# Optimization experiments

Measured on AMD Instinct MI355X. Metric: run time of the kernel, lower is better.

## Reference

```python
import jax, jax.numpy as jnp
import numpy as np

# Config matching init_kwargs / module defaults
B_T2I, B_LM, B_MMU = 2, 2, 2
B = B_T2I + B_LM + B_MMU
S = 1280
H, D = 16, 64
IMAGE_BE = [(128, 1152)]          # t2i_image_begin_end
MMU_END = 1027
PAD_BE = [(0, 80), (0, 100), (0, 110), (0, 0)]  # create_block_mask default pad_begin_ends


def _mixed_mask():
    """Vectorized translation of OmniAttentionMechanism.mixed_mask -> bool [B,S,S]."""
    q = jnp.arange(S)[:, None]    # [S,1] query index
    kv = jnp.arange(S)[None, :]   # [1,S] key index

    # t2i_full_begin / t2i_full_end (per-q image block bounds)
    full_begin = jnp.arange(S)
    full_end = jnp.arange(S)
    for ib, ie in IMAGE_BE:
        full_begin = full_begin.at[ib:ie].set(ib)
        full_end = full_end.at[ib:ie].set(ie)

    # pad_ends[b, kv]: arange baseline, first len(PAD_BE) batches get pad region end
    pad_ends = jnp.tile(jnp.arange(S)[None, :], (B, 1))
    for cnt, (pb, pe) in enumerate(PAD_BE):
        pad_ends = pad_ends.at[cnt, pb:pe].set(pe)

    # t2i: padded-causal OR bidirectional image block
    causal = (~(kv < pad_ends[:, None, :]) & (q >= kv)) | (q == kv)   # [B,S,S]
    full = (kv < full_end[:, None]) & (kv >= full_begin[:, None])     # [S,S] (q-indexed bounds)
    t2i = causal | full[None]
    lm = (q >= kv)[None]                                              # [1,S,S]
    mmu = ((q >= kv) | (kv < MMU_END))[None]                          # [1,S,S]

    b = jnp.arange(B)[:, None, None]
    # Faithful to the original XOR composition (terms are batch-disjoint so == OR)
    return ((b < B_T2I) & t2i) ^ ((b >= B_T2I) & (b < B_T2I + B_LM) & lm) ^ ((b >= B_T2I + B_LM) & mmu)


def setup_inputs() -> dict:
    key = jax.random.key(0)
    kq, kk, kv = jax.random.split(key, 3)
    shape = (B, H, S, D)
    return {
        "q": jax.random.normal(kq, shape, dtype=jnp.float32),
        "k": jax.random.normal(kk, shape, dtype=jnp.float32),
        "v": jax.random.normal(kv, shape, dtype=jnp.float32),
    }


def reference(q, k, v):
    """flex_attention(q, k, v, block_mask=mixed-t2i-lm-mmu) equivalent."""
    mask = _mixed_mask()[:, None]  # [B,1,S,S], broadcast over heads
    scale = 1.0 / jnp.sqrt(jnp.float32(D))  # flex_attention default scale
    scores = jnp.einsum('bhqd,bhkd->bhqk', q, k) * scale
    scores = jnp.where(mask, scores, -jnp.inf)  # every row has >=1 allowed key (q==kv / q>=kv)
    attn = jax.nn.softmax(scores, axis=-1)
    return jnp.einsum('bhqk,bhkd->bhqd', attn, v)
```

## Files before the change

### kernel.cpp

```cpp
#include <hip/hip_runtime.h>
#include <hip/hip_bf16.h>
#include <math.h>


#define SS 1280
#define DD 64
#define NH 16
#define TK 64
#define QB 128
#define NITEMS 960

typedef __attribute__((ext_vector_type(8))) short bf16x8;
typedef __attribute__((ext_vector_type(16))) float f32x16;

union UA { uint u[4]; bf16x8 v; };

__device__ inline uint pk2(float a, float b) {
    union { __hip_bfloat162 h; uint u; } cv;
    cv.h = __float22bfloat162_rn(float2{a, b});
    return cv.u;
}

__device__ inline void pl32(uint& a, uint& b) {
    asm volatile("v_permlane32_swap_b32 %0, %1" : "+v"(a), "+v"(b));
}

#define WAITVM4() asm volatile("s_waitcnt vmcnt(4)" ::: "memory")
#define WAITVM0() asm volatile("s_waitcnt vmcnt(0)" ::: "memory")

__device__ inline void decode_item(int i, int& b, int& h, int& qt) {
    if (i < 96)  { qt = 9; b = i / 16; h = i % 16; return; }
    i -= 96;
    if (i < 256) { b = i / 128; qt = 1 + (i % 128) / 16; h = i % 16; return; }
    i -= 256;
    if (i < 32)  { b = 2 + i / 16; qt = 8; h = i % 16; return; }
    i -= 32;
    if (i < 32)  { b = 4 + i / 16; qt = 8; h = i % 16; return; }
    i -= 32;
    if (i < 256) { b = 4 + i / 128; qt = (i % 128) / 16; h = i % 16; return; }
    i -= 256;
    if (i < 224) { qt = 7 - i / 32; b = 2 + (i % 32) / 16; h = i % 16; return; }
    i -= 224;
    if (i < 32)  { b = 2 + i / 16; qt = 0; h = i % 16; return; }
    i -= 32;
    b = i / 16; qt = 0; h = i % 16;
}

__global__ void zero_ctr_kernel(int* ctr) { if (threadIdx.x == 0) *ctr = 0; }

__global__ __launch_bounds__(256) void prepass8(
    const float* __restrict__ K, const float* __restrict__ V,
    ushort* __restrict__ Kb, ushort* __restrict__ Vtb)
{
    const int gx = blockIdx.x;
    const int t  = threadIdx.x;
    if (gx < 3840) {
        const size_t e = ((size_t)gx * 256 + t) * 8;
        const float4 a = *(const float4*)(K + e);
        const float4 c = *(const float4*)(K + e + 4);
        UA u;
        u.u[0] = pk2(a.x, a.y); u.u[1] = pk2(a.z, a.w);
        u.u[2] = pk2(c.x, c.y); u.u[3] = pk2(c.z, c.w);
        *(bf16x8*)(Kb + e) = u.v;
    } else {
        const int g   = gx - 3840;
        const int kvt = g % 20;
        const int p   = g / 20;
        __shared__ float T[64 * 67];
        const float* src = V + (size_t)p * (SS * DD) + (size_t)(kvt * 64) * DD;
#pragma unroll
        for (int i = 0; i < 16; ++i) {
            const int idx = t + 256 * i;
            T[(idx >> 6) * 67 + (idx & 63)] = src[idx];
        }
        __syncthreads();
        ushort* dst = Vtb + (size_t)p * (DD * SS) + kvt * 64;
#pragma unroll
        for (int i = 0; i < 2; ++i) {
            const int c0 = t + 256 * i;
            const int d = c0 >> 3, kc = c0 & 7;
            UA u;
#pragma unroll
            for (int j = 0; j < 4; ++j)
                u.u[j] = pk2(T[(kc * 8 + 2 * j) * 67 + d], T[(kc * 8 + 2 * j + 1) * 67 + d]);
            *(bf16x8*)(dst + (size_t)d * SS + kc * 8) = u.v;
        }
    }
}

__global__ __launch_bounds__(256) void omni_attn12(
    const float* __restrict__ Q, const ushort* __restrict__ Kb,
    const ushort* __restrict__ Vtb, float* __restrict__ O, int* __restrict__ ctr)
{
    const int t   = threadIdx.x;
    const int w   = t >> 6;
    const int l   = t & 63;
    const int l31 = l & 31;
    const int hi2 = l >> 5;

    __shared__ char smem[49152];
    __shared__ int s_item;

    const float scale = 0.125f * 1.44269504088896340736f;

    int koff[2], voff[2];
#pragma unroll
    for (int rd = 0; rd < 2; ++rd) {
        const int ci  = rd * 256 + w * 64 + l;
        const int row = ci >> 3, cc = ci & 7;
        koff[rd] = row * DD + (cc ^ (row & 7)) * 8;
        const int d = ci >> 3, vc = ci & 7;
        voff[rd] = d * SS + (vc ^ ((d ^ (d >> 3)) & 7)) * 8;
    }

    for (;;) {
        if (t == 0) s_item = atomicAdd(ctr, 1);
        __syncthreads();
        const int item = s_item;
        if (item >= NITEMS) break;

        int b, h, qt;
        decode_item(item, b, h, qt);
        const int p   = b * NH + h;
        const int qb0 = qt * QB;
        const int qw0 = qb0 + w * 32;
        const int qr  = qw0 + l31;
        const size_t pbase = (size_t)p * (SS * DD);

        const int bt = (b < 2) ? 0 : (b < 4) ? 1 : 2;
        const int pe = (b == 0) ? 80 : (b == 1) ? 100 : 0;
        const int qmax_blk = qb0 + QB - 1;
        const int qmax_w   = qw0 + 31;
        const bool blk_img = (qb0 + QB - 1 >= 128) && (qb0 < 1152);
        const bool w_img   = (qw0 >= 128) && (qw0 < 1152);

        bf16x8 qf[4];
#pragma unroll
        for (int ks = 0; ks < 4; ++ks) {
            const float* src = Q + pbase + (size_t)qr * DD + ks * 16 + hi2 * 8;
            const float4 a = *(const float4*)(src);
            const float4 c = *(const float4*)(src + 4);
            UA u;
            u.u[0] = pk2(a.x, a.y); u.u[1] = pk2(a.z, a.w);
            u.u[2] = pk2(c.x, c.y); u.u[3] = pk2(c.z, c.w);
            qf[ks] = u.v;
        }
        __builtin_amdgcn_sched_barrier(0);

        f32x16 o_acc[2];
#pragma unroll
        for (int ntd = 0; ntd < 2; ++ntd)
#pragma unroll
            for (int r = 0; r < 16; ++r) o_acc[ntd][r] = 0.f;
        float psum = 0.f;

        auto need_blk = [&](int k0) -> bool {
            if (bt == 0) return (k0 <= qmax_blk) || (blk_img && k0 >= 128 && k0 < 1152);
            if (bt == 1) return (k0 <= qmax_blk);
            return (k0 <= qmax_blk) || (k0 < 1027);
        };
        auto next_tile = [&](int k) -> int {
            k += TK;
            while (k < SS && !need_blk(k)) k += TK;
            return k;
        };
        auto stage = [&](int bsel, int k0) {
            char* buf = smem + bsel * 16384;
            const ushort* Kp = Kb + pbase + (size_t)k0 * DD;
            const ushort* Vp = Vtb + pbase + k0;
#pragma unroll
            for (int rd = 0; rd < 2; ++rd) {
                char* lb = buf + (rd * 256 + w * 64) * 16;
                __builtin_amdgcn_global_load_lds(
                    (const __attribute__((address_space(1))) void*)(Kp + koff[rd]),
                    (__attribute__((address_space(3))) void*)lb, 16, 0, 0);
            }
#pragma unroll
            for (int rd = 0; rd < 2; ++rd) {
                char* lb = buf + 8192 + (rd * 256 + w * 64) * 16;
                __builtin_amdgcn_global_load_lds(
                    (const __attribute__((address_space(1))) void*)(Vp + voff[rd]),
                    (__attribute__((address_space(3))) void*)lb, 16, 0, 0);
            }
        };

        int ka = 0, cur = 0;
        int kb = next_tile(0);
        int kc = (kb < SS) ? next_tile(kb) : SS;
        stage(0, ka);
        if (kb < SS) { stage(1, kb); WAITVM4(); } else { WAITVM0(); }
        __builtin_amdgcn_s_barrier();
        __builtin_amdgcn_sched_barrier(0);

        while (true) {
            if (kc < SS) stage((cur + 2) % 3, kc);

            char* cbuf = smem + cur * 16384;
            const int k0 = ka;
            const bool kv_img = (k0 >= 128) && (k0 < 1152);
            bool need_w, full_w;
            if (bt == 0) {
                need_w = (k0 <= qmax_w) || (w_img && kv_img);
                full_w = ((k0 >= pe) && (k0 + 63 <= qw0)) || (w_img && kv_img);
            } else if (bt == 1) {
                need_w = (k0 <= qmax_w);
                full_w = (k0 + 63 <= qw0);
            } else {
                need_w = (k0 <= qmax_w) || (k0 < 1027);
                full_w = (k0 + 63 <= qw0) || (k0 + 63 < 1027);
            }

            if (need_w) {
#pragma unroll
                for (int nt = 0; nt < 2; ++nt) {
                    f32x16 s;
#pragma unroll
                    for (int r = 0; r < 16; ++r) s[r] = 0.f;
                    __builtin_amdgcn_s_setprio(1);
#pragma unroll
                    for (int ksd = 0; ksd < 4; ++ksd) {
                        const int row = nt * 32 + l31;
                        int off = row * 128 + ksd * 32 + hi2 * 16;
                        off ^= (row & 7) << 4;
                        const bf16x8 kf = *(const bf16x8*)(cbuf + off);
                        s = __builtin_amdgcn_mfma_f32_32x32x16_bf16(kf, qf[ksd], s, 0, 0, 0);
                    }
                    __builtin_amdgcn_s_setprio(0);

                    const int c0 = k0 + nt * 32;
                    uint c[8];
#pragma unroll
                    for (int i = 0; i < 8; ++i) {
                        float pa, pb;
                        if (full_w) {
                            pa = __builtin_amdgcn_exp2f(s[2 * i] * scale);
                            pb = __builtin_amdgcn_exp2f(s[2 * i + 1] * scale);
                        } else {
                            const int r0i = 2 * i, r1i = 2 * i + 1;
                            const int kva = c0 + (r0i & 3) + 8 * (r0i >> 2) + 4 * hi2;
                            const int kvb = c0 + (r1i & 3) + 8 * (r1i >> 2) + 4 * hi2;
                            bool aa, ab;
                            if (bt == 0) {
                                aa = (qr == kva) | ((kva >= pe) & (qr >= kva)) |
                                     ((qr >= 128) & (qr < 1152) & (kva >= 128) & (kva < 1152));
                                ab = (qr == kvb) | ((kvb >= pe) & (qr >= kvb)) |
                                     ((qr >= 128) & (qr < 1152) & (kvb >= 128) & (kvb < 1152));
                            } else if (bt == 1) {
                                aa = (qr >= kva); ab = (qr >= kvb);
                            } else {
                                aa = (qr >= kva) | (kva < 1027);
                                ab = (qr >= kvb) | (kvb < 1027);
                            }
                            pa = aa ? __builtin_amdgcn_exp2f(s[2 * i] * scale) : 0.f;
                            pb = ab ? __builtin_amdgcn_exp2f(s[2 * i + 1] * scale) : 0.f;
                        }
                        psum += pa + pb;
                        c[i] = pk2(pa, pb);
                    }

                    UA A0, A1;
                    {
                        uint a0 = c[0], b0 = c[2]; pl32(a0, b0);
                        uint a1 = c[1], b1 = c[3]; pl32(a1, b1);
                        A0.u[0] = a0; A0.u[1] = a1; A0.u[2] = b0; A0.u[3] = b1;
                        uint a2 = c[4], b2 = c[6]; pl32(a2, b2);
                        uint a3 = c[5], b3 = c[7]; pl32(a3, b3);
                        A1.u[0] = a2; A1.u[1] = a3; A1.u[2] = b2; A1.u[3] = b3;
                    }

                    __builtin_amdgcn_s_setprio(1);
#pragma unroll
                    for (int ntd = 0; ntd < 2; ++ntd) {
                        const int row = ntd * 32 + l31;
                        const int swz = ((row ^ (row >> 3)) & 7) << 4;
                        int off0 = 8192 + row * 128 + (2 * nt) * 32 + hi2 * 16;     off0 ^= swz;
                        int off1 = 8192 + row * 128 + (2 * nt + 1) * 32 + hi2 * 16; off1 ^= swz;
                        const bf16x8 vf0 = *(const bf16x8*)(cbuf + off0);
                        o_acc[ntd] = __builtin_amdgcn_mfma_f32_32x32x16_bf16(A0.v, vf0, o_acc[ntd], 0, 0, 0);
                        const bf16x8 vf1 = *(const bf16x8*)(cbuf + off1);
                        o_acc[ntd] = __builtin_amdgcn_mfma_f32_32x32x16_bf16(A1.v, vf1, o_acc[ntd], 0, 0, 0);
                    }
                    __builtin_amdgcn_s_setprio(0);
                }
            }

            if (kc < SS) { WAITVM4(); } else { WAITVM0(); }
            __builtin_amdgcn_s_barrier();
            __builtin_amdgcn_sched_barrier(0);
            if (kb >= SS) break;
            ka = kb; kb = kc; kc = (kc < SS) ? next_tile(kc) : SS;
            cur = (cur + 1) % 3;
        }

        psum += __shfl_xor(psum, 32, 64);
#pragma unroll
        for (int r = 0; r < 16; ++r) {
            const int q_loc = (r & 3) + 8 * (r >> 2) + 4 * hi2;
            const float tv = __shfl(psum, q_loc, 64);
            const float iv = 1.f / tv;
            float* dst = O + pbase + (size_t)(qw0 + q_loc) * DD + l31;
#pragma unroll
            for (int ntd = 0; ntd < 2; ++ntd)
                dst[ntd * 32] = o_acc[ntd][r] * iv;
        }
    }
}

extern "C" void kernel_launch(void* const* d_in, const int* in_sizes, int n_in,
                              void* d_out, int out_size, void* d_ws, size_t ws_size,
                              hipStream_t stream) {
    const float* q = (const float*)d_in[0];
    const float* k = (const float*)d_in[1];
    const float* v = (const float*)d_in[2];
    float* o = (float*)d_out;

    const size_t NE = 7864320ULL;
    ushort* Kb  = (ushort*)d_ws;
    ushort* Vtb = Kb + NE;
    int* ctr    = (int*)((char*)d_ws + 2 * NE * sizeof(ushort));

    zero_ctr_kernel<<<1, 64, 0, stream>>>(ctr);
    prepass8<<<dim3(5760), 256, 0, stream>>>(k, v, Kb, Vtb);
    omni_attn12<<<dim3(768), 256, 0, stream>>>(q, Kb, Vtb, o, ctr);
}
```

Before: 114.8 us.

## Load V fragments directly to registers and drop persistent atomic scheduler

V tiles are now read straight from global memory into registers per wave, so LDS staging covers only K. This halves shared memory and adds occupancy hints (launch_bounds 256,4). The persistent work-stealing loop with its atomic counter and zero-init kernel is replaced by one block per work item in the same decode order, which also removes one kernel launch. The cost is more VGPRs for the V fragments and possibly less coalesced, higher-latency V loads. The pipeline also always issues a K stage, using a dummy tile at the end, to keep the vmcnt accounting uniform.

Result: slower. 143.0 us (+24.6%).

```diff
diff --git a/kernel.cpp b/kernel.cpp
--- a/kernel.cpp
+++ b/kernel.cpp
@@ -25,8 +25,7 @@
     asm volatile("v_permlane32_swap_b32 %0, %1" : "+v"(a), "+v"(b));
 }
 
-#define WAITVM4() asm volatile("s_waitcnt vmcnt(4)" ::: "memory")
-#define WAITVM0() asm volatile("s_waitcnt vmcnt(0)" ::: "memory")
+#define WAITVM2() asm volatile("s_waitcnt vmcnt(2)" ::: "memory")
 
 __device__ inline void decode_item(int i, int& b, int& h, int& qt) {
     if (i < 96)  { qt = 9; b = i / 16; h = i % 16; return; }
@@ -45,8 +44,6 @@
     i -= 32;
     b = i / 16; qt = 0; h = i % 16;
 }
-
-__global__ void zero_ctr_kernel(int* ctr) { if (threadIdx.x == 0) *ctr = 0; }
 
 __global__ __launch_bounds__(256) void prepass8(
     const float* __restrict__ K, const float* __restrict__ V,
@@ -67,11 +64,10 @@
         const int kvt = g % 20;
         const int p   = g / 20;
         __shared__ float T[64 * 67];
-        const float* src = V + (size_t)p * (SS * DD) + (size_t)(kvt * 64) * DD;
 #pragma unroll
         for (int i = 0; i < 16; ++i) {
             const int idx = t + 256 * i;
-            T[(idx >> 6) * 67 + (idx & 63)] = src[idx];
+            T[(idx >> 6) * 67 + (idx & 63)] = V[(size_t)p * (SS * DD) + (size_t)(kvt * 64) * DD + idx];
         }
         __syncthreads();
         ushort* dst = Vtb + (size_t)p * (DD * SS) + kvt * 64;
@@ -88,221 +84,213 @@
     }
 }
 
-__global__ __launch_bounds__(256) void omni_attn12(
+__global__ __launch_bounds__(256, 4) void omni_attn14(
     const float* __restrict__ Q, const ushort* __restrict__ Kb,
-    const ushort* __restrict__ Vtb, float* __restrict__ O, int* __restrict__ ctr)
+    const ushort* __restrict__ Vtb, float* __restrict__ O)
 {
+    int b, h, qt;
+    decode_item(blockIdx.x, b, h, qt);
+
     const int t   = threadIdx.x;
     const int w   = t >> 6;
     const int l   = t & 63;
     const int l31 = l & 31;
     const int hi2 = l >> 5;
 
-    __shared__ char smem[49152];
-    __shared__ int s_item;
+    const int p   = b * NH + h;
+    const int qb0 = qt * QB;
+    const int qw0 = qb0 + w * 32;
+    const int qr  = qw0 + l31;
+    const size_t pbase = (size_t)p * (SS * DD);
+
+    const int bt = (b < 2) ? 0 : (b < 4) ? 1 : 2;
+    const int pe = (b == 0) ? 80 : (b == 1) ? 100 : 0;
+    const int qmax_blk = qb0 + QB - 1;
+    const int qmax_w   = qw0 + 31;
+    const bool blk_img = (qb0 + QB - 1 >= 128) && (qb0 < 1152);
+    const bool w_img   = (qw0 >= 128) && (qw0 < 1152);
+
+    __shared__ char smem[3 * 8192];
 
     const float scale = 0.125f * 1.44269504088896340736f;
 
-    int koff[2], voff[2];
+    int koff[2];
 #pragma unroll
     for (int rd = 0; rd < 2; ++rd) {
         const int ci  = rd * 256 + w * 64 + l;
         const int row = ci >> 3, cc = ci & 7;
         koff[rd] = row * DD + (cc ^ (row & 7)) * 8;
-        const int d = ci >> 3, vc = ci & 7;
-        voff[rd] = d * SS + (vc ^ ((d ^ (d >> 3)) & 7)) * 8;
-    }
-
-    for (;;) {
-        if (t == 0) s_item = atomicAdd(ctr, 1);
-        __syncthreads();
-        const int item = s_item;
-        if (item >= NITEMS) break;
-
-        int b, h, qt;
-        decode_item(item, b, h, qt);
-        const int p   = b * NH + h;
-        const int qb0 = qt * QB;
-        const int qw0 = qb0 + w * 32;
-        const int qr  = qw0 + l31;
-        const size_t pbase = (size_t)p * (SS * DD);
-
-        const int bt = (b < 2) ? 0 : (b < 4) ? 1 : 2;
-        const int pe = (b == 0) ? 80 : (b == 1) ? 100 : 0;
-        const int qmax_blk = qb0 + QB - 1;
-        const int qmax_w   = qw0 + 31;
-        const bool blk_img = (qb0 + QB - 1 >= 128) && (qb0 < 1152);
-        const bool w_img   = (qw0 >= 128) && (qw0 < 1152);
-
-        bf16x8 qf[4];
-#pragma unroll
-        for (int ks = 0; ks < 4; ++ks) {
-            const float* src = Q + pbase + (size_t)qr * DD + ks * 16 + hi2 * 8;
-            const float4 a = *(const float4*)(src);
-            const float4 c = *(const float4*)(src + 4);
-            UA u;
-            u.u[0] = pk2(a.x, a.y); u.u[1] = pk2(a.z, a.w);
-            u.u[2] = pk2(c.x, c.y); u.u[3] = pk2(c.z, c.w);
-            qf[ks] = u.v;
-        }
-        __builtin_amdgcn_sched_barrier(0);
-
-        f32x16 o_acc[2];
-#pragma unroll
-        for (int ntd = 0; ntd < 2; ++ntd)
-#pragma unroll
-            for (int r = 0; r < 16; ++r) o_acc[ntd][r] = 0.f;
-        float psum = 0.f;
-
-        auto need_blk = [&](int k0) -> bool {
-            if (bt == 0) return (k0 <= qmax_blk) || (blk_img && k0 >= 128 && k0 < 1152);
-            if (bt == 1) return (k0 <= qmax_blk);
-            return (k0 <= qmax_blk) || (k0 < 1027);
-        };
-        auto next_tile = [&](int k) -> int {
-            k += TK;
-            while (k < SS && !need_blk(k)) k += TK;
-            return k;
-        };
-        auto stage = [&](int bsel, int k0) {
-            char* buf = smem + bsel * 16384;
-            const ushort* Kp = Kb + pbase + (size_t)k0 * DD;
-            const ushort* Vp = Vtb + pbase + k0;
-#pragma unroll
-            for (int rd = 0; rd < 2; ++rd) {
-                char* lb = buf + (rd * 256 + w * 64) * 16;
-                __builtin_amdgcn_global_load_lds(
-                    (const __attribute__((address_space(1))) void*)(Kp + koff[rd]),
-                    (__attribute__((address_space(3))) void*)lb, 16, 0, 0);
+    }
+
+    bf16x8 qf[4];
+#pragma unroll
+    for (int ks = 0; ks < 4; ++ks) {
+        const float* src = Q + pbase + (size_t)qr * DD + ks * 16 + hi2 * 8;
+        const float4 a = *(const float4*)(src);
+        const float4 c = *(const float4*)(src + 4);
+        UA u;
+        u.u[0] = pk2(a.x, a.y); u.u[1] = pk2(a.z, a.w);
+        u.u[2] = pk2(c.x, c.y); u.u[3] = pk2(c.z, c.w);
+        qf[ks] = u.v;
+    }
+
+    f32x16 o_acc[2];
+#pragma unroll
+    for (int ntd = 0; ntd < 2; ++ntd)
+#pragma unroll
+        for (int r = 0; r < 16; ++r) o_acc[ntd][r] = 0.f;
+    float psum = 0.f;
+
+    auto need_blk = [&](int k0) -> bool {
+        if (bt == 0) return (k0 <= qmax_blk) || (blk_img && k0 >= 128 && k0 < 1152);
+        if (bt == 1) return (k0 <= qmax_blk);
+        return (k0 <= qmax_blk) || (k0 < 1027);
+    };
+    auto next_tile = [&](int k) -> int {
+        k += TK;
+        while (k < SS && !need_blk(k)) k += TK;
+        return k;
+    };
+    auto stageK = [&](int bsel, int k0s) {
+        char* buf = smem + bsel * 8192;
+        const ushort* Kp = Kb + pbase + (size_t)k0s * DD;
+#pragma unroll
+        for (int rd = 0; rd < 2; ++rd) {
+            char* lb = buf + (rd * 256 + w * 64) * 16;
+            __builtin_amdgcn_global_load_lds(
+                (const __attribute__((address_space(1))) void*)(Kp + koff[rd]),
+                (__attribute__((address_space(3))) void*)lb, 16, 0, 0);
+        }
+    };
+
+    const ushort* vrow0 = Vtb + pbase + (size_t)l31 * SS + hi2 * 8;
+    const ushort* vrow1 = vrow0 + 32 * SS;
+
+    int ka = 0, cur = 0;
+    int kb = next_tile(0);
+    int kc = (kb < SS) ? next_tile(kb) : SS;
+    stageK(0, ka);
+    stageK(1, kb);
+    WAITVM2();
+    __builtin_amdgcn_s_barrier();
+    __builtin_amdgcn_sched_barrier(0);
+
+    while (true) {
+        const int k0 = ka;
+        const bool kv_img = (k0 >= 128) && (k0 < 1152);
+        bool need_w, full_w;
+        if (bt == 0) {
+            need_w = (k0 <= qmax_w) || (w_img && kv_img);
+            full_w = ((k0 >= pe) && (k0 + 63 <= qw0)) || (w_img && kv_img);
+        } else if (bt == 1) {
+            need_w = (k0 <= qmax_w);
+            full_w = (k0 + 63 <= qw0);
+        } else {
+            need_w = (k0 <= qmax_w) || (k0 < 1027);
+            full_w = (k0 + 63 <= qw0) || (k0 + 63 < 1027);
+        }
+
+        bf16x8 vf[8];
+        if (need_w) {
+            const ushort* v0 = vrow0 + k0;
+            const ushort* v1 = vrow1 + k0;
+#pragma unroll
+            for (int c4 = 0; c4 < 4; ++c4) vf[c4]     = *(const bf16x8*)(v0 + c4 * 16);
+#pragma unroll
+            for (int c4 = 0; c4 < 4; ++c4) vf[4 + c4] = *(const bf16x8*)(v1 + c4 * 16);
+        }
+
+        stageK((cur + 2) % 3, (kc < SS) ? kc : 0);
+
+        if (need_w) {
+            char* cbuf = smem + cur * 8192;
+#pragma unroll
+            for (int nt = 0; nt < 2; ++nt) {
+                f32x16 s;
+#pragma unroll
+                for (int r = 0; r < 16; ++r) s[r] = 0.f;
+                __builtin_amdgcn_s_setprio(1);
+#pragma unroll
+                for (int ksd = 0; ksd < 4; ++ksd) {
+                    const int row = nt * 32 + l31;
+                    int off = row * 128 + ksd * 32 + hi2 * 16;
+                    off ^= (row & 7) << 4;
+                    const bf16x8 kf = *(const bf16x8*)(cbuf + off);
+                    s = __builtin_amdgcn_mfma_f32_32x32x16_bf16(kf, qf[ksd], s, 0, 0, 0);
+                }
+                __builtin_amdgcn_s_setprio(0);
+
+                const int c0k = k0 + nt * 32;
+                uint c[8];
+#pragma unroll
+                for (int i = 0; i < 8; ++i) {
+                    float pa, pb;
+                    if (full_w) {
+                        pa = __builtin_amdgcn_exp2f(s[2 * i] * scale);
+                        pb = __builtin_amdgcn_exp2f(s[2 * i + 1] * scale);
+                    } else {
+                        const int r0i = 2 * i, r1i = 2 * i + 1;
+                        const int kva = c0k + (r0i & 3) + 8 * (r0i >> 2) + 4 * hi2;
+                        const int kvb = c0k + (r1i & 3) + 8 * (r1i >> 2) + 4 * hi2;
+                        bool aa, ab;
+                        if (bt == 0) {
+                            aa = (qr == kva) | ((kva >= pe) & (qr >= kva)) |
+                                 ((qr >= 128) & (qr < 1152) & (kva >= 128) & (kva < 1152));
+                            ab = (qr == kvb) | ((kvb >= pe) & (qr >= kvb)) |
+                                 ((qr >= 128) & (qr < 1152) & (kvb >= 128) & (kvb < 1152));
+                        } else if (bt == 1) {
+                            aa = (qr >= kva); ab = (qr >= kvb);
+                        } else {
+                            aa = (qr >= kva) | (kva < 1027);
+                            ab = (qr >= kvb) | (kvb < 1027);
+                        }
+                        pa = aa ? __builtin_amdgcn_exp2f(s[2 * i] * scale) : 0.f;
+                        pb = ab ? __builtin_amdgcn_exp2f(s[2 * i + 1] * scale) : 0.f;
+                    }
+                    psum += pa + pb;
+                    c[i] = pk2(pa, pb);
+                }
+
+                UA A0, A1;
+                {
+                    uint a0 = c[0], b0 = c[2]; pl32(a0, b0);
+                    uint a1 = c[1], b1 = c[3]; pl32(a1, b1);
+                    A0.u[0] = a0; A0.u[1] = a1; A0.u[2] = b0; A0.u[3] = b1;
+                    uint a2 = c[4], b2 = c[6]; pl32(a2, b2);
+                    uint a3 = c[5], b3 = c[7]; pl32(a3, b3);
+                    A1.u[0] = a2; A1.u[1] = a3; A1.u[2] = b2; A1.u[3] = b3;
+                }
+
+                __builtin_amdgcn_s_setprio(1);
+#pragma unroll
+                for (int ntd = 0; ntd < 2; ++ntd) {
+                    o_acc[ntd] = __builtin_amdgcn_mfma_f32_32x32x16_bf16(
+                        A0.v, vf[ntd * 4 + 2 * nt],     o_acc[ntd], 0, 0, 0);
+                    o_acc[ntd] = __builtin_amdgcn_mfma_f32_32x32x16_bf16(
+                        A1.v, vf[ntd * 4 + 2 * nt + 1], o_acc[ntd], 0, 0, 0);
+                }
+                __builtin_amdgcn_s_setprio(0);
             }
-#pragma unroll
-            for (int rd = 0; rd < 2; ++rd) {
-                char* lb = buf + 8192 + (rd * 256 + w * 64) * 16;
-                __builtin_amdgcn_global_load_lds(
-                    (const __attribute__((address_space(1))) void*)(Vp + voff[rd]),
-                    (__attribute__((address_space(3))) void*)lb, 16, 0, 0);
-            }
-        };
-
-        int ka = 0, cur = 0;
-        int kb = next_tile(0);
-        int kc = (kb < SS) ? next_tile(kb) : SS;
-        stage(0, ka);
-        if (kb < SS) { stage(1, kb); WAITVM4(); } else { WAITVM0(); }
+        }
+
+        WAITVM2();
         __builtin_amdgcn_s_barrier();
         __builtin_amdgcn_sched_barrier(0);
-
-        while (true) {
-            if (kc < SS) stage((cur + 2) % 3, kc);
-
-            char* cbuf = smem + cur * 16384;
-            const int k0 = ka;
-            const bool kv_img = (k0 >= 128) && (k0 < 1152);
-            bool need_w, full_w;
-            if (bt == 0) {
-                need_w = (k0 <= qmax_w) || (w_img && kv_img);
-                full_w = ((k0 >= pe) && (k0 + 63 <= qw0)) || (w_img && kv_img);
-            } else if (bt == 1) {
-                need_w = (k0 <= qmax_w);
-                full_w = (k0 + 63 <= qw0);
-            } else {
-                need_w = (k0 <= qmax_w) || (k0 < 1027);
-                full_w = (k0 + 63 <= qw0) || (k0 + 63 < 1027);
-            }
-
-            if (need_w) {
-#pragma unroll
-                for (int nt = 0; nt < 2; ++nt) {
-                    f32x16 s;
-#pragma unroll
-                    for (int r = 0; r < 16; ++r) s[r] = 0.f;
-                    __builtin_amdgcn_s_setprio(1);
-#pragma unroll
-                    for (int ksd = 0; ksd < 4; ++ksd) {
-                        const int row = nt * 32 + l31;
-                        int off = row * 128 + ksd * 32 + hi2 * 16;
-                        off ^= (row & 7) << 4;
-                        const bf16x8 kf = *(const bf16x8*)(cbuf + off);
-                        s = __builtin_amdgcn_mfma_f32_32x32x16_bf16(kf, qf[ksd], s, 0, 0, 0);
-                    }
-                    __builtin_amdgcn_s_setprio(0);
-
-                    const int c0 = k0 + nt * 32;
-                    uint c[8];
-#pragma unroll
-                    for (int i = 0; i < 8; ++i) {
-                        float pa, pb;
-                        if (full_w) {
-                            pa = __builtin_amdgcn_exp2f(s[2 * i] * scale);
-                            pb = __builtin_amdgcn_exp2f(s[2 * i + 1] * scale);
-                        } else {
-                            const int r0i = 2 * i, r1i = 2 * i + 1;
-                            const int kva = c0 + (r0i & 3) + 8 * (r0i >> 2) + 4 * hi2;
-                            const int kvb = c0 + (r1i & 3) + 8 * (r1i >> 2) + 4 * hi2;
-                            bool aa, ab;
-                            if (bt == 0) {
-                                aa = (qr == kva) | ((kva >= pe) & (qr >= kva)) |
-                                     ((qr >= 128) & (qr < 1152) & (kva >= 128) & (kva < 1152));
-                                ab = (qr == kvb) | ((kvb >= pe) & (qr >= kvb)) |
-                                     ((qr >= 128) & (qr < 1152) & (kvb >= 128) & (kvb < 1152));
-                            } else if (bt == 1) {
-                                aa = (qr >= kva); ab = (qr >= kvb);
-                            } else {
-                                aa = (qr >= kva) | (kva < 1027);
-                                ab = (qr >= kvb) | (kvb < 1027);
-                            }
-                            pa = aa ? __builtin_amdgcn_exp2f(s[2 * i] * scale) : 0.f;
-                            pb = ab ? __builtin_amdgcn_exp2f(s[2 * i + 1] * scale) : 0.f;
-                        }
-                        psum += pa + pb;
-                        c[i] = pk2(pa, pb);
-                    }
-
-                    UA A0, A1;
-                    {
-                        uint a0 = c[0], b0 = c[2]; pl32(a0, b0);
-                        uint a1 = c[1], b1 = c[3]; pl32(a1, b1);
-                        A0.u[0] = a0; A0.u[1] = a1; A0.u[2] = b0; A0.u[3] = b1;
-                        uint a2 = c[4], b2 = c[6]; pl32(a2, b2);
-                        uint a3 = c[5], b3 = c[7]; pl32(a3, b3);
-                        A1.u[0] = a2; A1.u[1] = a3; A1.u[2] = b2; A1.u[3] = b3;
-                    }
-
-                    __builtin_amdgcn_s_setprio(1);
-#pragma unroll
-                    for (int ntd = 0; ntd < 2; ++ntd) {
-                        const int row = ntd * 32 + l31;
-                        const int swz = ((row ^ (row >> 3)) & 7) << 4;
-                        int off0 = 8192 + row * 128 + (2 * nt) * 32 + hi2 * 16;     off0 ^= swz;
-                        int off1 = 8192 + row * 128 + (2 * nt + 1) * 32 + hi2 * 16; off1 ^= swz;
-                        const bf16x8 vf0 = *(const bf16x8*)(cbuf + off0);
-                        o_acc[ntd] = __builtin_amdgcn_mfma_f32_32x32x16_bf16(A0.v, vf0, o_acc[ntd], 0, 0, 0);
-                        const bf16x8 vf1 = *(const bf16x8*)(cbuf + off1);
-                        o_acc[ntd] = __builtin_amdgcn_mfma_f32_32x32x16_bf16(A1.v, vf1, o_acc[ntd], 0, 0, 0);
-                    }
-                    __builtin_amdgcn_s_setprio(0);
-                }
-            }
-
-            if (kc < SS) { WAITVM4(); } else { WAITVM0(); }
-            __builtin_amdgcn_s_barrier();
-            __builtin_amdgcn_sched_barrier(0);
-            if (kb >= SS) break;
-            ka = kb; kb = kc; kc = (kc < SS) ? next_tile(kc) : SS;
-            cur = (cur + 1) % 3;
-        }
-
-        psum += __shfl_xor(psum, 32, 64);
-#pragma unroll
-        for (int r = 0; r < 16; ++r) {
-            const int q_loc = (r & 3) + 8 * (r >> 2) + 4 * hi2;
-            const float tv = __shfl(psum, q_loc, 64);
-            const float iv = 1.f / tv;
-            float* dst = O + pbase + (size_t)(qw0 + q_loc) * DD + l31;
-#pragma unroll
-            for (int ntd = 0; ntd < 2; ++ntd)
-                dst[ntd * 32] = o_acc[ntd][r] * iv;
-        }
+        if (kb >= SS) break;
+        ka = kb; kb = kc; kc = (kc < SS) ? next_tile(kc) : SS;
+        cur = (cur + 1) % 3;
+    }
+
+    psum += __shfl_xor(psum, 32, 64);
+#pragma unroll
+    for (int r = 0; r < 16; ++r) {
+        const int q_loc = (r & 3) + 8 * (r >> 2) + 4 * hi2;
+        const float tv = __shfl(psum, q_loc, 64);
+        const float iv = 1.f / tv;
+        float* dst = O + pbase + (size_t)(qw0 + q_loc) * DD + l31;
+#pragma unroll
+        for (int ntd = 0; ntd < 2; ++ntd)
+            dst[ntd * 32] = o_acc[ntd][r] * iv;
     }
 }
 
@@ -317,9 +305,7 @@
     const size_t NE = 7864320ULL;
     ushort* Kb  = (ushort*)d_ws;
     ushort* Vtb = Kb + NE;
-    int* ctr    = (int*)((char*)d_ws + 2 * NE * sizeof(ushort));
-
-    zero_ctr_kernel<<<1, 64, 0, stream>>>(ctr);
+
     prepass8<<<dim3(5760), 256, 0, stream>>>(k, v, Kb, Vtb);
-    omni_attn12<<<dim3(768), 256, 0, stream>>>(q, Kb, Vtb, o, ctr);
-}
+    omni_attn14<<<dim3(NITEMS), 256, 0, stream>>>(q, Kb, Vtb, o);
+}
```
